# Kernel tuning notes

Hardware: AMD Instinct MI355X
Metric: run time of the kernel (lower is better)

Reference implementation:

```python
import jax, jax.numpy as jnp
import numpy as np

TQ, T, D = 2048, 16384, 256
H, KD, VD, DOUT = 8, 32, 32, 256


def setup_inputs() -> dict:
    key = jax.random.key(0)
    ks = jax.random.split(key, 8)
    w_scale = 1.0 / np.sqrt(D)
    return {
        "query": jax.random.normal(ks[0], (TQ, D), dtype=jnp.float32),
        "key": jax.random.normal(ks[1], (T, D), dtype=jnp.float32),
        "value": jax.random.normal(ks[2], (T, D), dtype=jnp.float32),
        "wq": jax.random.normal(ks[3], (D, H * KD), dtype=jnp.float32) * w_scale,
        "bq": jnp.zeros((H * KD,), dtype=jnp.float32),
        "wk": jax.random.normal(ks[4], (D, H * KD), dtype=jnp.float32) * w_scale,
        "bk": jnp.zeros((H * KD,), dtype=jnp.float32),
        "wv": jax.random.normal(ks[5], (D, H * VD), dtype=jnp.float32) * w_scale,
        "bv": jnp.zeros((H * VD,), dtype=jnp.float32),
        "wo": jax.random.normal(ks[6], (H * VD, DOUT), dtype=jnp.float32) * (1.0 / np.sqrt(H * VD)),
        "bo": jnp.zeros((DOUT,), dtype=jnp.float32),
    }


def reference(query, key, value, wq, bq, wk, bk, wv, bv, wo, bo):
    # Linear projections to heads: [Tq,H,KD], [T,H,KD], [T,H,VD]
    qh = (query @ wq + bq).reshape(TQ, H, KD)
    kh = (key @ wk + bk).reshape(T, H, KD)
    vh = (value @ wv + bv).reshape(T, H, VD)
    # Chunked online-softmax attention == exact softmax attention.
    # Query scaled by 1/sqrt(head_dim) as in the memory-efficient impl.
    scale = np.float32(1.0 / np.sqrt(KD))
    logits = jnp.einsum("qhd,khd->hqk", qh * scale, kh)  # [H,Tq,T]
    weights = jax.nn.softmax(logits, axis=-1)
    attn = jnp.einsum("hqk,khd->qhd", weights, vh).reshape(TQ, H * VD)
    return attn @ wo + bo  # [Tq, DOUT]
```

## Files before the change

### kernel.cpp

```cpp
#include <hip/hip_runtime.h>
#include <stdint.h>


typedef float f32x4 __attribute__((ext_vector_type(4)));
typedef __bf16 bf16x8 __attribute__((ext_vector_type(8)));

__device__ __forceinline__ unsigned short f2bf(float f) {
  unsigned int u = __builtin_bit_cast(unsigned int, f);
  u += 0x7FFFu + ((u >> 16) & 1u);
  return (unsigned short)(u >> 16);
}

__device__ __forceinline__ f32x4 mfma16(bf16x8 a, bf16x8 b, f32x4 c) {
  return __builtin_amdgcn_mfma_f32_16x16x32_bf16(a, b, c, 0, 0, 0);
}

__device__ __forceinline__ float ex2(float x) {
#if __has_builtin(__builtin_amdgcn_exp2f)
  return __builtin_amdgcn_exp2f(x);
#else
  return exp2f(x);
#endif
}

#define QSCALE 0.25503483f

__global__ __launch_bounds__(256) void convert_w_kernel(
    const float* __restrict__ wq, const float* __restrict__ wk,
    const float* __restrict__ wv, const float* __restrict__ wo,
    unsigned short* __restrict__ tq, unsigned short* __restrict__ tk,
    unsigned short* __restrict__ tv, unsigned short* __restrict__ to)
{
  const int mat = blockIdx.x >> 6, k0 = (blockIdx.x & 63) * 4, n = threadIdx.x;
  const float* src; unsigned short* dst;
  if (mat == 0) { src = wq; dst = tq; }
  else if (mat == 1) { src = wk; dst = tk; }
  else if (mat == 2) { src = wv; dst = tv; }
  else { src = wo; dst = to; }
  unsigned e0 = f2bf(src[(size_t)(k0 + 0) * 256 + n]);
  unsigned e1 = f2bf(src[(size_t)(k0 + 1) * 256 + n]);
  unsigned e2 = f2bf(src[(size_t)(k0 + 2) * 256 + n]);
  unsigned e3 = f2bf(src[(size_t)(k0 + 3) * 256 + n]);
  uint2 pk = { e0 | (e1 << 16), e2 | (e3 << 16) };
  *(uint2*)&dst[(size_t)n * 256 + k0] = pk;
}

__global__ __launch_bounds__(256) void proj3_kernel(
    const float* __restrict__ X, const unsigned short* __restrict__ Wt,
    const float* __restrict__ bias, unsigned short* __restrict__ out,
    int N, float scale, int vmode)
{
  const int tid = threadIdx.x;
  const int w = tid >> 6, lane = tid & 63, g = lane >> 4, c = lane & 15;
  const int m0 = blockIdx.x * 64, cb = blockIdx.y * 128;

  __shared__ __align__(16) unsigned short Xs[64 * 40];
  __shared__ __align__(16) unsigned short Ws2[128 * 40];

  const f32x4 zero4 = {0.f, 0.f, 0.f, 0.f};
  f32x4 acc[4][2];
  #pragma unroll
  for (int i = 0; i < 4; ++i) { acc[i][0] = zero4; acc[i][1] = zero4; }

  const int srow = tid >> 2, sks = (tid & 3) * 8;
  const int wrow = tid >> 1, wseg = (tid & 1) * 16;

  for (int k0 = 0; k0 < 256; k0 += 32) {
    if (k0) __syncthreads();
    {
      const float* xp = X + (size_t)(m0 + srow) * 256 + k0 + sks;
      float4 x0 = *(const float4*)xp;
      float4 x1 = *(const float4*)(xp + 4);
      int4 pk;
      pk.x = (int)f2bf(x0.x) | ((int)f2bf(x0.y) << 16);
      pk.y = (int)f2bf(x0.z) | ((int)f2bf(x0.w) << 16);
      pk.z = (int)f2bf(x1.x) | ((int)f2bf(x1.y) << 16);
      pk.w = (int)f2bf(x1.z) | ((int)f2bf(x1.w) << 16);
      *(int4*)&Xs[srow * 40 + sks] = pk;
    }
    {
      const unsigned short* wp = Wt + (size_t)(cb + wrow) * 256 + k0 + wseg;
      int4 w0 = *(const int4*)wp;
      int4 w1 = *(const int4*)(wp + 8);
      *(int4*)&Ws2[wrow * 40 + wseg] = w0;
      *(int4*)&Ws2[wrow * 40 + wseg + 8] = w1;
    }
    __syncthreads();

    bf16x8 a[4], b[2];
    #pragma unroll
    for (int rt = 0; rt < 4; ++rt)
      a[rt] = *(const bf16x8*)&Xs[(16 * rt + c) * 40 + 8 * g];
    #pragma unroll
    for (int ct = 0; ct < 2; ++ct)
      b[ct] = *(const bf16x8*)&Ws2[(32 * w + 16 * ct + c) * 40 + 8 * g];
    #pragma unroll
    for (int rt = 0; rt < 4; ++rt)
      #pragma unroll
      for (int ct = 0; ct < 2; ++ct)
        acc[rt][ct] = mfma16(a[rt], b[ct], acc[rt][ct]);
  }

  #pragma unroll
  for (int ct = 0; ct < 2; ++ct) {
    const int col = cb + 32 * w + 16 * ct + c;
    const float bv = bias[col];
    const int hh = col >> 5, d = col & 31;
    #pragma unroll
    for (int rt = 0; rt < 4; ++rt)
      #pragma unroll
      for (int r = 0; r < 4; ++r) {
        const int row = m0 + 16 * rt + 4 * g + r;
        const unsigned short v = f2bf((acc[rt][ct][r] + bv) * scale);
        if (vmode) {
          const int pr = (row & ~31) | (((row >> 3) & 1) << 4) |
                         (((row >> 2) & 1) << 3) | (((row >> 4) & 1) << 2) |
                         (row & 3);
          out[((size_t)hh * 32 + d) * (size_t)N + pr] = v;
        } else {
          out[((size_t)hh * N + row) * 32 + d] = v;
        }
      }
  }
}

__global__ __launch_bounds__(256) void attn3_kernel(
    const unsigned short* __restrict__ qh, const unsigned short* __restrict__ kh,
    const unsigned short* __restrict__ vth,
    float* __restrict__ part_o, float* __restrict__ part_l)
{
  const int qb = blockIdx.x, h = blockIdx.y, sp = blockIdx.z;
  const int tid = threadIdx.x;
  const int w = tid >> 6, lane = tid & 63, g = lane >> 4, c = lane & 15;
  const int q0 = qb * 64 + w * 16;

  __shared__ __align__(16) unsigned short Ks[64 * 40];
  __shared__ __align__(16) unsigned short Vt[32 * 72];

  const bf16x8 qf = *(const bf16x8*)&qh[((size_t)h * 2048 + q0 + c) * 32 + 8 * g];

  const f32x4 zero4 = {0.f, 0.f, 0.f, 0.f};
  f32x4 acc0 = zero4, acc1 = zero4;
  float l = 0.f;

  const int skey = tid >> 2, sseg = (tid & 3) * 8;
  const int kwoff = skey * 40 + sseg;
  const int vrow = tid >> 3, vseg = (tid & 7) * 8;
  const int vwoff = vrow * 72 + vseg;

  const unsigned short* kp = kh + (size_t)h * 524288 +
                             ((size_t)(sp * 4096) + skey) * 32 + sseg;
  const unsigned short* vp = vth + ((size_t)h * 32 + vrow) * 16384 +
                             sp * 4096 + vseg;

  int4 kA = *(const int4*)kp;  int4 vA = *(const int4*)vp;
  kp += 2048; vp += 64;
  int4 kB, vB;

  auto compute = [&]() {
    bf16x8 kf0 = *(const bf16x8*)&Ks[(c) * 40 + 8 * g];
    bf16x8 kf1 = *(const bf16x8*)&Ks[(16 + c) * 40 + 8 * g];
    bf16x8 kf2 = *(const bf16x8*)&Ks[(32 + c) * 40 + 8 * g];
    bf16x8 kf3 = *(const bf16x8*)&Ks[(48 + c) * 40 + 8 * g];
    f32x4 s0 = mfma16(kf0, qf, zero4);
    f32x4 s1 = mfma16(kf1, qf, zero4);
    f32x4 s2 = mfma16(kf2, qf, zero4);
    f32x4 s3 = mfma16(kf3, qf, zero4);
    bf16x8 v00 = *(const bf16x8*)&Vt[c * 72 + 8 * g];
    bf16x8 v01 = *(const bf16x8*)&Vt[c * 72 + 32 + 8 * g];
    bf16x8 v10 = *(const bf16x8*)&Vt[(16 + c) * 72 + 8 * g];
    bf16x8 v11 = *(const bf16x8*)&Vt[(16 + c) * 72 + 32 + 8 * g];
    float rs = 0.f;
    union { __bf16 b[8]; bf16x8 v; } pa0, pa1;
    #pragma unroll
    for (int r = 0; r < 4; ++r) {
      float p0 = ex2(s0[r]), p1 = ex2(s1[r]);
      float p2 = ex2(s2[r]), p3 = ex2(s3[r]);
      rs += (p0 + p1) + (p2 + p3);
      pa0.b[r] = (__bf16)p0; pa0.b[4 + r] = (__bf16)p1;
      pa1.b[r] = (__bf16)p2; pa1.b[4 + r] = (__bf16)p3;
    }
    rs += __shfl_xor(rs, 16);
    rs += __shfl_xor(rs, 32);
    l += rs;
    acc0 = mfma16(v00, pa0.v, acc0);
    acc1 = mfma16(v10, pa0.v, acc1);
    acc0 = mfma16(v01, pa1.v, acc0);
    acc1 = mfma16(v11, pa1.v, acc1);
  };

  for (int dit = 0; dit < 32; ++dit) {
    __syncthreads();
    *(int4*)&Ks[kwoff] = kA;
    *(int4*)&Vt[vwoff] = vA;
    kB = *(const int4*)kp;  vB = *(const int4*)vp;
    __syncthreads();
    compute();
    __syncthreads();
    *(int4*)&Ks[kwoff] = kB;
    *(int4*)&Vt[vwoff] = vB;
    {
      const int ka = (dit < 31) ? 2048 : 0;
      const int va = (dit < 31) ? 64 : 0;
      kA = *(const int4*)(kp + ka);  vA = *(const int4*)(vp + va);
    }
    kp += 4096; vp += 128;
    __syncthreads();
    compute();
  }

  float* po = part_o + ((size_t)((sp * 8 + h) * 2048) + q0 + c) * 32;
  #pragma unroll
  for (int r = 0; r < 4; ++r) {
    po[4 * g + r]      = acc0[r];
    po[16 + 4 * g + r] = acc1[r];
  }
  if (lane < 16)
    part_l[(size_t)((sp * 8 + h) * 2048) + q0 + lane] = l;
}

__global__ __launch_bounds__(256) void combine3_kernel(
    const float* __restrict__ part_o, const float* __restrict__ part_l,
    unsigned short* __restrict__ attnb)
{
  const int gid = blockIdx.x * 256 + threadIdx.x;
  const int d = gid & 31, q = (gid >> 5) & 2047, h = gid >> 16;
  float L = 0.f, o = 0.f;
  #pragma unroll
  for (int s = 0; s < 4; ++s) {
    L += part_l[(size_t)((s * 8 + h) * 2048) + q];
    o += part_o[((size_t)((s * 8 + h) * 2048) + q) * 32 + d];
  }
  attnb[(size_t)q * 256 + h * 32 + d] = f2bf(o / L);
}

__global__ __launch_bounds__(256) void oproj3_kernel(
    const unsigned short* __restrict__ A, const unsigned short* __restrict__ Wt,
    const float* __restrict__ bias, float* __restrict__ out)
{
  const int tid = threadIdx.x;
  const int w = tid >> 6, lane = tid & 63, g = lane >> 4, c = lane & 15;
  const int m0 = blockIdx.x * 64, cb = blockIdx.y * 128;

  __shared__ __align__(16) unsigned short As[64 * 40];
  __shared__ __align__(16) unsigned short Ws2[128 * 40];

  const f32x4 zero4 = {0.f, 0.f, 0.f, 0.f};
  f32x4 acc[4][2];
  #pragma unroll
  for (int i = 0; i < 4; ++i) { acc[i][0] = zero4; acc[i][1] = zero4; }

  const int arow = tid >> 2, aseg = (tid & 3) * 8;
  const int wrow = tid >> 1, wseg = (tid & 1) * 16;

  for (int k0 = 0; k0 < 256; k0 += 32) {
    if (k0) __syncthreads();
    *(int4*)&As[arow * 40 + aseg] =
        *(const int4*)&A[(size_t)(m0 + arow) * 256 + k0 + aseg];
    {
      const unsigned short* wp = Wt + (size_t)(cb + wrow) * 256 + k0 + wseg;
      int4 w0 = *(const int4*)wp;
      int4 w1 = *(const int4*)(wp + 8);
      *(int4*)&Ws2[wrow * 40 + wseg] = w0;
      *(int4*)&Ws2[wrow * 40 + wseg + 8] = w1;
    }
    __syncthreads();

    bf16x8 a[4], b[2];
    #pragma unroll
    for (int rt = 0; rt < 4; ++rt)
      a[rt] = *(const bf16x8*)&As[(16 * rt + c) * 40 + 8 * g];
    #pragma unroll
    for (int ct = 0; ct < 2; ++ct)
      b[ct] = *(const bf16x8*)&Ws2[(32 * w + 16 * ct + c) * 40 + 8 * g];
    #pragma unroll
    for (int rt = 0; rt < 4; ++rt)
      #pragma unroll
      for (int ct = 0; ct < 2; ++ct)
        acc[rt][ct] = mfma16(a[rt], b[ct], acc[rt][ct]);
  }

  #pragma unroll
  for (int ct = 0; ct < 2; ++ct) {
    const int col = cb + 32 * w + 16 * ct + c;
    const float bv = bias[col];
    #pragma unroll
    for (int rt = 0; rt < 4; ++rt)
      #pragma unroll
      for (int r = 0; r < 4; ++r)
        out[(size_t)(m0 + 16 * rt + 4 * g + r) * 256 + col] = acc[rt][ct][r] + bv;
  }
}

extern "C" void kernel_launch(void* const* d_in, const int* in_sizes, int n_in,
                              void* d_out, int out_size, void* d_ws, size_t ws_size,
                              hipStream_t stream)
{
  (void)in_sizes; (void)n_in; (void)out_size; (void)ws_size;
  const float* query = (const float*)d_in[0];
  const float* key   = (const float*)d_in[1];
  const float* value = (const float*)d_in[2];
  const float* wq    = (const float*)d_in[3];
  const float* bq    = (const float*)d_in[4];
  const float* wk    = (const float*)d_in[5];
  const float* bk    = (const float*)d_in[6];
  const float* wv    = (const float*)d_in[7];
  const float* bv    = (const float*)d_in[8];
  const float* wo    = (const float*)d_in[9];
  const float* bo    = (const float*)d_in[10];
  float* out = (float*)d_out;

  unsigned char* ws = (unsigned char*)d_ws;
  unsigned short* qh    = (unsigned short*)(ws);
  unsigned short* khp   = (unsigned short*)(ws + 1048576);
  unsigned short* vtp   = (unsigned short*)(ws + 9437184);
  unsigned short* attnb = (unsigned short*)(ws + 17825792);
  float* part_o = (float*)(ws + 18874368);
  unsigned short* wtq = (unsigned short*)(ws + 18874368);
  unsigned short* wtk = (unsigned short*)(ws + 19005440);
  unsigned short* wtv = (unsigned short*)(ws + 19136512);
  float* part_l = (float*)(ws + 27262976);
  unsigned short* wto = (unsigned short*)(ws + 27525120);

  convert_w_kernel<<<256, 256, 0, stream>>>(wq, wk, wv, wo, wtq, wtk, wtv, wto);
  proj3_kernel<<<dim3(32, 2),  256, 0, stream>>>(query, wtq, bq, qh,  2048,  QSCALE, 0);
  proj3_kernel<<<dim3(256, 2), 256, 0, stream>>>(key,   wtk, bk, khp, 16384, 1.0f,   0);
  proj3_kernel<<<dim3(256, 2), 256, 0, stream>>>(value, wtv, bv, vtp, 16384, 1.0f,   1);
  attn3_kernel<<<dim3(32, 8, 4), 256, 0, stream>>>(qh, khp, vtp, part_o, part_l);
  combine3_kernel<<<2048, 256, 0, stream>>>(part_o, part_l, attnb);
  oproj3_kernel<<<dim3(32, 2), 256, 0, stream>>>(attnb, wto, bo, out);
}
```

Measured before the change: 117.0 us.

## Merge projections, retile attention with double-buffered LDS, fuse combine into output projection

The three Q/K/V projection launches become one 512-thread launch that covers all 256 output columns per block. The attention kernel now has each wave handle 32 queries, splits the keys 8 ways, double-buffers K/V in LDS with one barrier per tile, remaps block order, raises priority around the PV MFMAs, and writes bf16 partial outputs. The combine kernel is removed: the output projection sums the 8 partials and normalises while staging its A tile. This cuts launches and intermediate traffic, at the cost of bf16 rounding on partial sums and more split overhead.

```diff
diff --git a/kernel.cpp b/kernel.cpp
--- a/kernel.cpp
+++ b/kernel.cpp
@@ -10,17 +10,24 @@
   u += 0x7FFFu + ((u >> 16) & 1u);
   return (unsigned short)(u >> 16);
 }
-
+__device__ __forceinline__ float bf2f(unsigned u) {
+  return __builtin_bit_cast(float, u << 16);
+}
 __device__ __forceinline__ f32x4 mfma16(bf16x8 a, bf16x8 b, f32x4 c) {
   return __builtin_amdgcn_mfma_f32_16x16x32_bf16(a, b, c, 0, 0, 0);
 }
-
 __device__ __forceinline__ float ex2(float x) {
 #if __has_builtin(__builtin_amdgcn_exp2f)
   return __builtin_amdgcn_exp2f(x);
 #else
   return exp2f(x);
 #endif
+}
+__device__ __forceinline__ uint2 pack4(f32x4 a) {
+  uint2 r;
+  r.x = (unsigned)f2bf(a[0]) | ((unsigned)f2bf(a[1]) << 16);
+  r.y = (unsigned)f2bf(a[2]) | ((unsigned)f2bf(a[3]) << 16);
+  return r;
 }
 
 #define QSCALE 0.25503483f
@@ -45,45 +52,56 @@
   *(uint2*)&dst[(size_t)n * 256 + k0] = pk;
 }
 
-__global__ __launch_bounds__(256) void proj3_kernel(
-    const float* __restrict__ X, const unsigned short* __restrict__ Wt,
-    const float* __restrict__ bias, unsigned short* __restrict__ out,
-    int N, float scale, int vmode)
-{
+__global__ __launch_bounds__(512) void proj4_kernel(
+    const float* __restrict__ Xq, const float* __restrict__ Xk,
+    const float* __restrict__ Xv,
+    const unsigned short* __restrict__ Wtq, const unsigned short* __restrict__ Wtk,
+    const unsigned short* __restrict__ Wtv,
+    const float* __restrict__ Bq, const float* __restrict__ Bk,
+    const float* __restrict__ Bv,
+    unsigned short* __restrict__ Oq, unsigned short* __restrict__ Ok,
+    unsigned short* __restrict__ Ov)
+{
+  const int mat = blockIdx.y;
+  const float* X; const unsigned short* Wt; const float* Bp; unsigned short* Op;
+  int N; float scale; int vmode;
+  if (mat == 0) {
+    if (blockIdx.x >= 32) return;
+    X = Xq; Wt = Wtq; Bp = Bq; Op = Oq; N = 2048; scale = QSCALE; vmode = 0;
+  } else if (mat == 1) {
+    X = Xk; Wt = Wtk; Bp = Bk; Op = Ok; N = 16384; scale = 1.f; vmode = 0;
+  } else {
+    X = Xv; Wt = Wtv; Bp = Bv; Op = Ov; N = 16384; scale = 1.f; vmode = 1;
+  }
   const int tid = threadIdx.x;
   const int w = tid >> 6, lane = tid & 63, g = lane >> 4, c = lane & 15;
-  const int m0 = blockIdx.x * 64, cb = blockIdx.y * 128;
+  const int m0 = blockIdx.x * 64;
 
   __shared__ __align__(16) unsigned short Xs[64 * 40];
-  __shared__ __align__(16) unsigned short Ws2[128 * 40];
+  __shared__ __align__(16) unsigned short Ws[256 * 40];
 
   const f32x4 zero4 = {0.f, 0.f, 0.f, 0.f};
   f32x4 acc[4][2];
   #pragma unroll
   for (int i = 0; i < 4; ++i) { acc[i][0] = zero4; acc[i][1] = zero4; }
 
-  const int srow = tid >> 2, sks = (tid & 3) * 8;
+  const int xrow = tid >> 3, xseg = (tid & 7) * 4;
   const int wrow = tid >> 1, wseg = (tid & 1) * 16;
 
   for (int k0 = 0; k0 < 256; k0 += 32) {
     if (k0) __syncthreads();
     {
-      const float* xp = X + (size_t)(m0 + srow) * 256 + k0 + sks;
-      float4 x0 = *(const float4*)xp;
-      float4 x1 = *(const float4*)(xp + 4);
-      int4 pk;
-      pk.x = (int)f2bf(x0.x) | ((int)f2bf(x0.y) << 16);
-      pk.y = (int)f2bf(x0.z) | ((int)f2bf(x0.w) << 16);
-      pk.z = (int)f2bf(x1.x) | ((int)f2bf(x1.y) << 16);
-      pk.w = (int)f2bf(x1.z) | ((int)f2bf(x1.w) << 16);
-      *(int4*)&Xs[srow * 40 + sks] = pk;
+      float4 x = *(const float4*)&X[(size_t)(m0 + xrow) * 256 + k0 + xseg];
+      uint2 px = { (unsigned)f2bf(x.x) | ((unsigned)f2bf(x.y) << 16),
+                   (unsigned)f2bf(x.z) | ((unsigned)f2bf(x.w) << 16) };
+      *(uint2*)&Xs[xrow * 40 + xseg] = px;
     }
     {
-      const unsigned short* wp = Wt + (size_t)(cb + wrow) * 256 + k0 + wseg;
+      const unsigned short* wp = Wt + (size_t)wrow * 256 + k0 + wseg;
       int4 w0 = *(const int4*)wp;
       int4 w1 = *(const int4*)(wp + 8);
-      *(int4*)&Ws2[wrow * 40 + wseg] = w0;
-      *(int4*)&Ws2[wrow * 40 + wseg + 8] = w1;
+      *(int4*)&Ws[wrow * 40 + wseg] = w0;
+      *(int4*)&Ws[wrow * 40 + wseg + 8] = w1;
     }
     __syncthreads();
 
@@ -93,7 +111,7 @@
       a[rt] = *(const bf16x8*)&Xs[(16 * rt + c) * 40 + 8 * g];
     #pragma unroll
     for (int ct = 0; ct < 2; ++ct)
-      b[ct] = *(const bf16x8*)&Ws2[(32 * w + 16 * ct + c) * 40 + 8 * g];
+      b[ct] = *(const bf16x8*)&Ws[(32 * w + 16 * ct + c) * 40 + 8 * g];
     #pragma unroll
     for (int rt = 0; rt < 4; ++rt)
       #pragma unroll
@@ -103,8 +121,8 @@
 
   #pragma unroll
   for (int ct = 0; ct < 2; ++ct) {
-    const int col = cb + 32 * w + 16 * ct + c;
-    const float bv = bias[col];
+    const int col = 32 * w + 16 * ct + c;
+    const float bv = Bp[col];
     const int hh = col >> 5, d = col & 31;
     #pragma unroll
     for (int rt = 0; rt < 4; ++rt)
@@ -116,32 +134,36 @@
           const int pr = (row & ~31) | (((row >> 3) & 1) << 4) |
                          (((row >> 2) & 1) << 3) | (((row >> 4) & 1) << 2) |
                          (row & 3);
-          out[((size_t)hh * 32 + d) * (size_t)N + pr] = v;
+          Op[((size_t)hh * 32 + d) * (size_t)N + pr] = v;
         } else {
-          out[((size_t)hh * N + row) * 32 + d] = v;
+          Op[((size_t)hh * N + row) * 32 + d] = v;
         }
       }
   }
 }
 
-__global__ __launch_bounds__(256) void attn3_kernel(
+__global__ __launch_bounds__(256) void attn4_kernel(
     const unsigned short* __restrict__ qh, const unsigned short* __restrict__ kh,
     const unsigned short* __restrict__ vth,
-    float* __restrict__ part_o, float* __restrict__ part_l)
-{
-  const int qb = blockIdx.x, h = blockIdx.y, sp = blockIdx.z;
+    unsigned short* __restrict__ part_o, float* __restrict__ part_l)
+{
+  const int f = blockIdx.x + 16 * (blockIdx.y + 8 * blockIdx.z);
+  const int v = (f & 7) * 128 + (f >> 3);
+  const int qb = v & 15, h = (v >> 4) & 7, sp = v >> 7;
+
   const int tid = threadIdx.x;
   const int w = tid >> 6, lane = tid & 63, g = lane >> 4, c = lane & 15;
-  const int q0 = qb * 64 + w * 16;
-
-  __shared__ __align__(16) unsigned short Ks[64 * 40];
-  __shared__ __align__(16) unsigned short Vt[32 * 72];
-
-  const bf16x8 qf = *(const bf16x8*)&qh[((size_t)h * 2048 + q0 + c) * 32 + 8 * g];
+  const int q0 = qb * 128 + w * 32;
+
+  __shared__ __align__(16) unsigned short Ks[2][64 * 40];
+  __shared__ __align__(16) unsigned short Vt[2][32 * 72];
+
+  const bf16x8 qf0 = *(const bf16x8*)&qh[((size_t)h * 2048 + q0 + c) * 32 + 8 * g];
+  const bf16x8 qf1 = *(const bf16x8*)&qh[((size_t)h * 2048 + q0 + 16 + c) * 32 + 8 * g];
 
   const f32x4 zero4 = {0.f, 0.f, 0.f, 0.f};
-  f32x4 acc0 = zero4, acc1 = zero4;
-  float l = 0.f;
+  f32x4 acc00 = zero4, acc01 = zero4, acc10 = zero4, acc11 = zero4;
+  float l0 = 0.f, l1 = 0.f;
 
   const int skey = tid >> 2, sseg = (tid & 3) * 8;
   const int kwoff = skey * 40 + sseg;
@@ -149,120 +171,145 @@
   const int vwoff = vrow * 72 + vseg;
 
   const unsigned short* kp = kh + (size_t)h * 524288 +
-                             ((size_t)(sp * 4096) + skey) * 32 + sseg;
+                             ((size_t)(sp * 2048) + skey) * 32 + sseg;
   const unsigned short* vp = vth + ((size_t)h * 32 + vrow) * 16384 +
-                             sp * 4096 + vseg;
-
-  int4 kA = *(const int4*)kp;  int4 vA = *(const int4*)vp;
-  kp += 2048; vp += 64;
-  int4 kB, vB;
-
-  auto compute = [&]() {
-    bf16x8 kf0 = *(const bf16x8*)&Ks[(c) * 40 + 8 * g];
-    bf16x8 kf1 = *(const bf16x8*)&Ks[(16 + c) * 40 + 8 * g];
-    bf16x8 kf2 = *(const bf16x8*)&Ks[(32 + c) * 40 + 8 * g];
-    bf16x8 kf3 = *(const bf16x8*)&Ks[(48 + c) * 40 + 8 * g];
-    f32x4 s0 = mfma16(kf0, qf, zero4);
-    f32x4 s1 = mfma16(kf1, qf, zero4);
-    f32x4 s2 = mfma16(kf2, qf, zero4);
-    f32x4 s3 = mfma16(kf3, qf, zero4);
-    bf16x8 v00 = *(const bf16x8*)&Vt[c * 72 + 8 * g];
-    bf16x8 v01 = *(const bf16x8*)&Vt[c * 72 + 32 + 8 * g];
-    bf16x8 v10 = *(const bf16x8*)&Vt[(16 + c) * 72 + 8 * g];
-    bf16x8 v11 = *(const bf16x8*)&Vt[(16 + c) * 72 + 32 + 8 * g];
-    float rs = 0.f;
-    union { __bf16 b[8]; bf16x8 v; } pa0, pa1;
+                             sp * 2048 + vseg;
+
+  int4 kA = *(const int4*)kp;
+  int4 vA = *(const int4*)vp;
+  *(int4*)&Ks[0][kwoff] = kA;
+  *(int4*)&Vt[0][vwoff] = vA;
+  kA = *(const int4*)(kp + 2048);
+  vA = *(const int4*)(vp + 64);
+  __syncthreads();
+
+  for (int it = 0; it < 32; ++it) {
+    const int cur = it & 1;
+    if (it < 31) {
+      *(int4*)&Ks[cur ^ 1][kwoff] = kA;
+      *(int4*)&Vt[cur ^ 1][vwoff] = vA;
+      const int t2 = (it + 2) & 31;
+      kA = *(const int4*)(kp + t2 * 2048);
+      vA = *(const int4*)(vp + t2 * 64);
+    }
+
+    const unsigned short* Kb = &Ks[cur][0];
+    const unsigned short* Vb = &Vt[cur][0];
+    bf16x8 kf0 = *(const bf16x8*)&Kb[(c) * 40 + 8 * g];
+    bf16x8 kf1 = *(const bf16x8*)&Kb[(16 + c) * 40 + 8 * g];
+    bf16x8 kf2 = *(const bf16x8*)&Kb[(32 + c) * 40 + 8 * g];
+    bf16x8 kf3 = *(const bf16x8*)&Kb[(48 + c) * 40 + 8 * g];
+
+    f32x4 s0 = mfma16(kf0, qf0, zero4);
+    f32x4 s1 = mfma16(kf1, qf0, zero4);
+    f32x4 s2 = mfma16(kf2, qf0, zero4);
+    f32x4 s3 = mfma16(kf3, qf0, zero4);
+    union { __bf16 b[8]; bf16x8 v; } pa00, pa01, pa10, pa11;
+    float rs0 = 0.f;
     #pragma unroll
     for (int r = 0; r < 4; ++r) {
       float p0 = ex2(s0[r]), p1 = ex2(s1[r]);
       float p2 = ex2(s2[r]), p3 = ex2(s3[r]);
-      rs += (p0 + p1) + (p2 + p3);
-      pa0.b[r] = (__bf16)p0; pa0.b[4 + r] = (__bf16)p1;
-      pa1.b[r] = (__bf16)p2; pa1.b[4 + r] = (__bf16)p3;
-    }
-    rs += __shfl_xor(rs, 16);
-    rs += __shfl_xor(rs, 32);
-    l += rs;
-    acc0 = mfma16(v00, pa0.v, acc0);
-    acc1 = mfma16(v10, pa0.v, acc1);
-    acc0 = mfma16(v01, pa1.v, acc0);
-    acc1 = mfma16(v11, pa1.v, acc1);
-  };
-
-  for (int dit = 0; dit < 32; ++dit) {
+      rs0 += (p0 + p1) + (p2 + p3);
+      pa00.b[r] = (__bf16)p0; pa00.b[4 + r] = (__bf16)p1;
+      pa01.b[r] = (__bf16)p2; pa01.b[4 + r] = (__bf16)p3;
+    }
+    rs0 += __shfl_xor(rs0, 16);
+    rs0 += __shfl_xor(rs0, 32);
+    l0 += rs0;
+    s0 = mfma16(kf0, qf1, zero4);
+    s1 = mfma16(kf1, qf1, zero4);
+    s2 = mfma16(kf2, qf1, zero4);
+    s3 = mfma16(kf3, qf1, zero4);
+    float rs1 = 0.f;
+    #pragma unroll
+    for (int r = 0; r < 4; ++r) {
+      float p0 = ex2(s0[r]), p1 = ex2(s1[r]);
+      float p2 = ex2(s2[r]), p3 = ex2(s3[r]);
+      rs1 += (p0 + p1) + (p2 + p3);
+      pa10.b[r] = (__bf16)p0; pa10.b[4 + r] = (__bf16)p1;
+      pa11.b[r] = (__bf16)p2; pa11.b[4 + r] = (__bf16)p3;
+    }
+    rs1 += __shfl_xor(rs1, 16);
+    rs1 += __shfl_xor(rs1, 32);
+    l1 += rs1;
+
+    bf16x8 v00 = *(const bf16x8*)&Vb[c * 72 + 8 * g];
+    bf16x8 v01 = *(const bf16x8*)&Vb[c * 72 + 32 + 8 * g];
+    bf16x8 v10 = *(const bf16x8*)&Vb[(16 + c) * 72 + 8 * g];
+    bf16x8 v11 = *(const bf16x8*)&Vb[(16 + c) * 72 + 32 + 8 * g];
+    __builtin_amdgcn_s_setprio(1);
+    acc00 = mfma16(v00, pa00.v, acc00);
+    acc01 = mfma16(v10, pa00.v, acc01);
+    acc00 = mfma16(v01, pa01.v, acc00);
+    acc01 = mfma16(v11, pa01.v, acc01);
+    acc10 = mfma16(v00, pa10.v, acc10);
+    acc11 = mfma16(v10, pa10.v, acc11);
+    acc10 = mfma16(v01, pa11.v, acc10);
+    acc11 = mfma16(v11, pa11.v, acc11);
+    __builtin_amdgcn_s_setprio(0);
+
     __syncthreads();
-    *(int4*)&Ks[kwoff] = kA;
-    *(int4*)&Vt[vwoff] = vA;
-    kB = *(const int4*)kp;  vB = *(const int4*)vp;
-    __syncthreads();
-    compute();
-    __syncthreads();
-    *(int4*)&Ks[kwoff] = kB;
-    *(int4*)&Vt[vwoff] = vB;
-    {
-      const int ka = (dit < 31) ? 2048 : 0;
-      const int va = (dit < 31) ? 64 : 0;
-      kA = *(const int4*)(kp + ka);  vA = *(const int4*)(vp + va);
-    }
-    kp += 4096; vp += 128;
-    __syncthreads();
-    compute();
-  }
-
-  float* po = part_o + ((size_t)((sp * 8 + h) * 2048) + q0 + c) * 32;
-  #pragma unroll
-  for (int r = 0; r < 4; ++r) {
-    po[4 * g + r]      = acc0[r];
-    po[16 + 4 * g + r] = acc1[r];
-  }
-  if (lane < 16)
-    part_l[(size_t)((sp * 8 + h) * 2048) + q0 + lane] = l;
-}
-
-__global__ __launch_bounds__(256) void combine3_kernel(
-    const float* __restrict__ part_o, const float* __restrict__ part_l,
-    unsigned short* __restrict__ attnb)
-{
-  const int gid = blockIdx.x * 256 + threadIdx.x;
-  const int d = gid & 31, q = (gid >> 5) & 2047, h = gid >> 16;
-  float L = 0.f, o = 0.f;
-  #pragma unroll
-  for (int s = 0; s < 4; ++s) {
-    L += part_l[(size_t)((s * 8 + h) * 2048) + q];
-    o += part_o[((size_t)((s * 8 + h) * 2048) + q) * 32 + d];
-  }
-  attnb[(size_t)q * 256 + h * 32 + d] = f2bf(o / L);
-}
-
-__global__ __launch_bounds__(256) void oproj3_kernel(
-    const unsigned short* __restrict__ A, const unsigned short* __restrict__ Wt,
-    const float* __restrict__ bias, float* __restrict__ out)
+  }
+
+  const size_t pbase = (size_t)(sp * 8 + h) * 2048;
+  unsigned short* po0 = part_o + (pbase + q0 + c) * 32;
+  *(uint2*)&po0[4 * g]      = pack4(acc00);
+  *(uint2*)&po0[16 + 4 * g] = pack4(acc01);
+  unsigned short* po1 = part_o + (pbase + q0 + 16 + c) * 32;
+  *(uint2*)&po1[4 * g]      = pack4(acc10);
+  *(uint2*)&po1[16 + 4 * g] = pack4(acc11);
+  if (lane < 16) {
+    part_l[pbase + q0 + lane]      = l0;
+    part_l[pbase + q0 + 16 + lane] = l1;
+  }
+}
+
+__global__ __launch_bounds__(512) void oproj4_kernel(
+    const unsigned short* __restrict__ part_o, const float* __restrict__ part_l,
+    const unsigned short* __restrict__ Wt, const float* __restrict__ bias,
+    float* __restrict__ out)
 {
   const int tid = threadIdx.x;
   const int w = tid >> 6, lane = tid & 63, g = lane >> 4, c = lane & 15;
-  const int m0 = blockIdx.x * 64, cb = blockIdx.y * 128;
+  const int m0 = blockIdx.x * 64;
 
   __shared__ __align__(16) unsigned short As[64 * 40];
-  __shared__ __align__(16) unsigned short Ws2[128 * 40];
+  __shared__ __align__(16) unsigned short Ws[256 * 40];
 
   const f32x4 zero4 = {0.f, 0.f, 0.f, 0.f};
   f32x4 acc[4][2];
   #pragma unroll
   for (int i = 0; i < 4; ++i) { acc[i][0] = zero4; acc[i][1] = zero4; }
 
-  const int arow = tid >> 2, aseg = (tid & 3) * 8;
+  const int arow = tid >> 3, aseg = (tid & 7) * 4;
   const int wrow = tid >> 1, wseg = (tid & 1) * 16;
 
   for (int k0 = 0; k0 < 256; k0 += 32) {
+    const int h = k0 >> 5;
     if (k0) __syncthreads();
-    *(int4*)&As[arow * 40 + aseg] =
-        *(const int4*)&A[(size_t)(m0 + arow) * 256 + k0 + aseg];
     {
-      const unsigned short* wp = Wt + (size_t)(cb + wrow) * 256 + k0 + wseg;
+      float L = 0.f;
+      float o0 = 0.f, o1 = 0.f, o2 = 0.f, o3 = 0.f;
+      #pragma unroll
+      for (int s = 0; s < 8; ++s) {
+        const size_t b = (size_t)(s * 8 + h) * 2048 + m0 + arow;
+        L += part_l[b];
+        uint2 pk = *(const uint2*)&part_o[b * 32 + aseg];
+        o0 += bf2f(pk.x & 0xffffu); o1 += bf2f(pk.x >> 16);
+        o2 += bf2f(pk.y & 0xffffu); o3 += bf2f(pk.y >> 16);
+      }
+      const float inv = 1.f / L;
+      uint2 pa = { (unsigned)f2bf(o0 * inv) | ((unsigned)f2bf(o1 * inv) << 16),
+                   (unsigned)f2bf(o2 * inv) | ((unsigned)f2bf(o3 * inv) << 16) };
+      *(uint2*)&As[arow * 40 + aseg] = pa;
+    }
+    {
+      const unsigned short* wp = Wt + (size_t)wrow * 256 + k0 + wseg;
       int4 w0 = *(const int4*)wp;
       int4 w1 = *(const int4*)(wp + 8);
-      *(int4*)&Ws2[wrow * 40 + wseg] = w0;
-      *(int4*)&Ws2[wrow * 40 + wseg + 8] = w1;
+      *(int4*)&Ws[wrow * 40 + wseg] = w0;
+      *(int4*)&Ws[wrow * 40 + wseg + 8] = w1;
     }
     __syncthreads();
 
@@ -272,7 +319,7 @@
       a[rt] = *(const bf16x8*)&As[(16 * rt + c) * 40 + 8 * g];
     #pragma unroll
     for (int ct = 0; ct < 2; ++ct)
-      b[ct] = *(const bf16x8*)&Ws2[(32 * w + 16 * ct + c) * 40 + 8 * g];
+      b[ct] = *(const bf16x8*)&Ws[(32 * w + 16 * ct + c) * 40 + 8 * g];
     #pragma unroll
     for (int rt = 0; rt < 4; ++rt)
       #pragma unroll
@@ -282,7 +329,7 @@
 
   #pragma unroll
   for (int ct = 0; ct < 2; ++ct) {
-    const int col = cb + 32 * w + 16 * ct + c;
+    const int col = 32 * w + 16 * ct + c;
     const float bv = bias[col];
     #pragma unroll
     for (int rt = 0; rt < 4; ++rt)
@@ -311,22 +358,19 @@
   float* out = (float*)d_out;
 
   unsigned char* ws = (unsigned char*)d_ws;
-  unsigned short* qh    = (unsigned short*)(ws);
-  unsigned short* khp   = (unsigned short*)(ws + 1048576);
-  unsigned short* vtp   = (unsigned short*)(ws + 9437184);
-  unsigned short* attnb = (unsigned short*)(ws + 17825792);
-  float* part_o = (float*)(ws + 18874368);
-  unsigned short* wtq = (unsigned short*)(ws + 18874368);
-  unsigned short* wtk = (unsigned short*)(ws + 19005440);
-  unsigned short* wtv = (unsigned short*)(ws + 19136512);
-  float* part_l = (float*)(ws + 27262976);
-  unsigned short* wto = (unsigned short*)(ws + 27525120);
+  unsigned short* qh     = (unsigned short*)(ws);
+  unsigned short* khp    = (unsigned short*)(ws + 1048576);
+  unsigned short* vtp    = (unsigned short*)(ws + 9437184);
+  unsigned short* part_o = (unsigned short*)(ws + 17825792);
+  unsigned short* wtq    = (unsigned short*)(ws + 17825792);
+  unsigned short* wtk    = (unsigned short*)(ws + 17956864);
+  unsigned short* wtv    = (unsigned short*)(ws + 18087936);
+  float*          part_l = (float*)(ws + 26214400);
+  unsigned short* wto    = (unsigned short*)(ws + 26738688);
 
   convert_w_kernel<<<256, 256, 0, stream>>>(wq, wk, wv, wo, wtq, wtk, wtv, wto);
-  proj3_kernel<<<dim3(32, 2),  256, 0, stream>>>(query, wtq, bq, qh,  2048,  QSCALE, 0);
-  proj3_kernel<<<dim3(256, 2), 256, 0, stream>>>(key,   wtk, bk, khp, 16384, 1.0f,   0);
-  proj3_kernel<<<dim3(256, 2), 256, 0, stream>>>(value, wtv, bv, vtp, 16384, 1.0f,   1);
-  attn3_kernel<<<dim3(32, 8, 4), 256, 0, stream>>>(qh, khp, vtp, part_o, part_l);
-  combine3_kernel<<<2048, 256, 0, stream>>>(part_o, part_l, attnb);
-  oproj3_kernel<<<dim3(32, 2), 256, 0, stream>>>(attnb, wto, bo, out);
-}
+  proj4_kernel<<<dim3(256, 3), 512, 0, stream>>>(
+      query, key, value, wtq, wtk, wtv, bq, bk, bv, qh, khp, vtp);
+  attn4_kernel<<<dim3(16, 8, 8), 256, 0, stream>>>(qh, khp, vtp, part_o, part_l);
+  oproj4_kernel<<<32, 512, 0, stream>>>(part_o, part_l, wto, bo, out);
+}
```

Result: faster. 111.6 us (-4.7%).
